# Optimization experiments

Hardware: AMD Instinct MI355X
Metric: run time of the kernel (lower is better)

## Reference

```python
import jax, jax.numpy as jnp
import numpy as np

# Model hyperparameters (match init_kwargs)
G = 256      # graph_size
K = 6        # conv kernel size
CH = 8       # channels
ROWS = 4
COLS = 3
B = 64       # batch
H = G - K + 1  # conv output side (square) = 251


def setup_inputs() -> dict:
    key = jax.random.key(0)
    k1, k2, k3, k4 = jax.random.split(key, 4)
    x = jax.random.normal(k1, (B, G, G), dtype=jnp.float32)
    # Conv2d(1, CH, (K,K)) weights, kaiming_normal_ (fan_in = 1*K*K, gain=sqrt(2))
    fan_in = 1 * K * K
    conv_w = jax.random.normal(k2, (CH, 1, K, K), dtype=jnp.float32) * np.float32(np.sqrt(2.0 / fan_in))
    # torch Conv2d default bias init: U(-1/sqrt(fan_in), 1/sqrt(fan_in))
    bound = np.float32(1.0 / np.sqrt(fan_in))
    conv_b = jax.random.uniform(k3, (CH,), dtype=jnp.float32, minval=-bound, maxval=bound)
    # coef parameter [CH, ROWS, COLS], kaiming_normal_ (fan_in = ROWS*COLS)
    coef = jax.random.normal(k4, (CH, ROWS, COLS), dtype=jnp.float32) * np.float32(np.sqrt(2.0 / (ROWS * COLS)))
    return {"x": x, "conv_w": conv_w, "conv_b": conv_b, "coef": coef}


def _traces_of_powers(C):
    """C: [H,H]. Returns traces of C^(i+2) for i in 0..ROWS-1 (matches torch loop:
    x_series[0]=C@C; at step i it records trace(x_series[i]) = trace(C^(i+2))."""
    def step(P, _):
        return C @ P, jnp.trace(P)
    _, ts = jax.lax.scan(step, C @ C, None, length=ROWS)
    return ts  # [ROWS]


def reference(x, conv_w, conv_b, coef):
    # conv over each sample treated as [1,1,G,G] -> vectorized as [B,1,G,G]
    y = jax.lax.conv_general_dilated(
        x[:, None], conv_w, window_strides=(1, 1), padding='VALID',
        dimension_numbers=('NCHW', 'OIHW', 'NCHW'))
    y = y + conv_b[None, :, None, None]           # [B, CH, H, H]

    ts = jax.vmap(jax.vmap(_traces_of_powers))(y)  # [B, CH, ROWS]

    jpow = jnp.arange(1, COLS + 1, dtype=jnp.float32)            # exponents j+1
    ret = ts[..., None] ** jpow                                  # [B, CH, ROWS, COLS]
    numel = jnp.float32(H * H)
    exps = (jnp.arange(ROWS, dtype=jnp.float32)[:, None]
            + jnp.arange(COLS, dtype=jnp.float32)[None, :] + 1.0)  # i+j+1
    ret = ret / (numel ** exps)                                  # [B, CH, ROWS, COLS]

    terms = coef[None] * ret
    return terms.sum(axis=(1, 2, 3))  # [B]
```

## Files before the change

### kernel.cpp

```cpp
#include <hip/hip_runtime.h>

typedef short short8 __attribute__((ext_vector_type(8)));
typedef float f32x4 __attribute__((ext_vector_type(4)));

#define B_    64
#define CH_   8
#define NBC   512
#define MATU  65536
#define H_    251
#define PADX  73
#define LDSW  40

__device__ inline unsigned short bf16r(float f){
    unsigned u = __float_as_uint(f);
    u += 0x7fffu + ((u >> 16) & 1u);
    return (unsigned short)(u >> 16);
}
__device__ inline float bf16f(unsigned short h){ return __uint_as_float(((unsigned)h) << 16); }
__device__ inline unsigned packsplit(float v){
    unsigned short h = bf16r(v);
    unsigned short l = bf16r(v - bf16f(h));
    return (((unsigned)h) << 16) | (unsigned)l;
}
__device__ inline float unpackf(unsigned u){
    return __uint_as_float(u & 0xffff0000u) + bf16f((unsigned short)(u & 0xffffu));
}

__global__ __launch_bounds__(256) void conv_pack(const float* __restrict__ x,
                                                 const float* __restrict__ w,
                                                 const float* __restrict__ bias,
                                                 unsigned* __restrict__ Ypk,
                                                 int b_base) {
    __shared__ float xt[69 * PADX];
    __shared__ float wsm[76];

    int tid = threadIdx.x;
    int tile = blockIdx.x;
    int lb = blockIdx.y;
    int cp = blockIdx.z;
    int b = b_base + lb;
    int r0 = (tile >> 2) * 64, c0 = (tile & 3) * 64;

    if (tid < 72) wsm[tid] = w[cp * 72 + tid];
    if (tid < 2)  wsm[72 + tid] = bias[cp * 2 + tid];

    const float* xb = x + (size_t)b * 65536;
    for (int idx = tid; idx < 69 * PADX; idx += 256) {
        int row = idx / PADX, col = idx - row * PADX;
        float v = 0.f;
        if (col < 69) {
            int gr = r0 + row; if (gr > 255) gr = 255;
            int gc = c0 + col; if (gc > 255) gc = 255;
            v = xb[gr * 256 + gc];
        }
        xt[idx] = v;
    }
    __syncthreads();

    int tx = tid & 15, ty = tid >> 4;

    for (int cc = 0; cc < 2; ++cc) {
        int ch = cp * 2 + cc;
        float acc[4][4];
        float bv = wsm[72 + cc];
        #pragma unroll
        for (int i = 0; i < 4; ++i)
            #pragma unroll
            for (int j = 0; j < 4; ++j) acc[i][j] = bv;

        const float* wc = &wsm[cc * 36];
        #pragma unroll
        for (int ir = 0; ir < 9; ++ir) {
            float row[9];
            #pragma unroll
            for (int c = 0; c < 9; ++c) row[c] = xt[(ty * 4 + ir) * PADX + tx * 4 + c];
            #pragma unroll
            for (int i = 0; i < 4; ++i) {
                int u = ir - i;
                if (u >= 0 && u < 6) {
                    #pragma unroll
                    for (int v = 0; v < 6; ++v) {
                        float wv = wc[u * 6 + v];
                        #pragma unroll
                        for (int j = 0; j < 4; ++j) acc[i][j] += row[j + v] * wv;
                    }
                }
            }
        }

        unsigned pk[4][4];
        #pragma unroll
        for (int i = 0; i < 4; ++i) {
            int gr = r0 + ty * 4 + i;
            #pragma unroll
            for (int j = 0; j < 4; ++j) {
                int gc = c0 + tx * 4 + j;
                float v = (gr < H_ && gc < H_) ? acc[i][j] : 0.f;
                pk[i][j] = packsplit(v);
            }
        }

        unsigned* yrow = Ypk + (size_t)(lb * 8 + ch) * MATU;
        #pragma unroll
        for (int i = 0; i < 4; ++i) {
            uint4 v = make_uint4(pk[i][0], pk[i][1], pk[i][2], pk[i][3]);
            *(uint4*)&yrow[(size_t)(r0 + ty * 4 + i) * 256 + c0 + tx * 4] = v;
        }
    }
}

template<int PHASE>
__global__ __launch_bounds__(256) void gemm_mfma(const unsigned* __restrict__ Apk,
                                                 const unsigned* __restrict__ Ypk,
                                                 unsigned* __restrict__ Mpk,
                                                 double* __restrict__ pdiag,
                                                 double* __restrict__ pfull,
                                                 int bc_base, int cur) {
    __shared__ __align__(16) char smem[53248];
    __shared__ double redbuf[8];

    unsigned short* Ahi = (unsigned short*)smem;
    unsigned short* Alo = (unsigned short*)(smem + 10240);
    unsigned short* Bhi = (unsigned short*)(smem + 20480);
    unsigned short* Blo = (unsigned short*)(smem + 36864);

    int tid = threadIdx.x;

    int hw = blockIdx.x;
    int xcd = hw & 7, s = hw >> 3;
    int mpx = cur >> 3;
    int lbc = xcd * mpx + (s >> 2);
    int t4 = s & 3;
    int by = t4 >> 1, bx = t4 & 1;
    int bi = by * 128, bj = bx * 128;
    int bc = bc_base + lbc;

    const unsigned* A = Apk + (size_t)lbc * MATU;

    int wid = tid >> 6, l = tid & 63;
    int wr = wid >> 1, wc = wid & 1;
    int l15 = l & 15, lk = l >> 4;

    f32x4 acc[4][4];
    #pragma unroll
    for (int m = 0; m < 4; ++m)
        #pragma unroll
        for (int n = 0; n < 4; ++n) acc[m][n] = (f32x4){0.f, 0.f, 0.f, 0.f};

    const int cl  = tid & 31;
    const int grp = tid >> 5;
    const int kq  = grp * 4;
    const int kb  = grp >> 1;
    const int koff = (grp & 1) * 4;

    for (int k0 = 0; k0 < 256; k0 += 32) {
        #pragma unroll
        for (int p = 0; p < 4; ++p) {
            int g = p * 256 + tid;
            int row = g >> 3, chn = g & 7;
            uint4 qa = *(const uint4*)(A + (size_t)(bi + row) * 256 + k0 + chn * 4);
            *(ushort4*)&Ahi[row * LDSW + chn * 4] =
                make_ushort4(qa.x >> 16, qa.y >> 16, qa.z >> 16, qa.w >> 16);
            *(ushort4*)&Alo[row * LDSW + chn * 4] =
                make_ushort4(qa.x & 0xffff, qa.y & 0xffff, qa.z & 0xffff, qa.w & 0xffff);
        }
        {
            const unsigned* Bp = A + (size_t)(k0 + kq) * 256 + bj + cl;
            unsigned d[4][4];
            #pragma unroll
            for (int i = 0; i < 4; ++i)
                #pragma unroll
                for (int j = 0; j < 4; ++j)
                    d[i][j] = Bp[i * 256 + j * 32];
            #pragma unroll
            for (int j = 0; j < 4; ++j) {
                int c = cl + 32 * j;
                *(ushort4*)&Bhi[kb * 1024 + c * 8 + koff] =
                    make_ushort4(d[0][j] >> 16, d[1][j] >> 16, d[2][j] >> 16, d[3][j] >> 16);
                *(ushort4*)&Blo[kb * 1024 + c * 8 + koff] =
                    make_ushort4(d[0][j] & 0xffff, d[1][j] & 0xffff, d[2][j] & 0xffff, d[3][j] & 0xffff);
            }
        }
        __syncthreads();

        short8 ah[4], al[4], bh[4], bl[4];
        #pragma unroll
        for (int m = 0; m < 4; ++m) {
            int r = wr * 64 + m * 16 + l15;
            ah[m] = *(const short8*)&Ahi[r * LDSW + lk * 8];
            al[m] = *(const short8*)&Alo[r * LDSW + lk * 8];
        }
        #pragma unroll
        for (int n = 0; n < 4; ++n) {
            int c = wc * 64 + n * 16 + l15;
            bh[n] = *(const short8*)&Bhi[lk * 1024 + c * 8];
            bl[n] = *(const short8*)&Blo[lk * 1024 + c * 8];
        }
        #pragma unroll
        for (int m = 0; m < 4; ++m)
            #pragma unroll
            for (int n = 0; n < 4; ++n) {
                acc[m][n] = __builtin_amdgcn_mfma_f32_16x16x32_bf16(ah[m], bh[n], acc[m][n], 0, 0, 0);
                acc[m][n] = __builtin_amdgcn_mfma_f32_16x16x32_bf16(ah[m], bl[n], acc[m][n], 0, 0, 0);
                acc[m][n] = __builtin_amdgcn_mfma_f32_16x16x32_bf16(al[m], bh[n], acc[m][n], 0, 0, 0);
            }
        __syncthreads();
    }

    const unsigned* Yb = Ypk + (size_t)lbc * MATU;
    unsigned* Mw = (PHASE == 1) ? (Mpk + (size_t)lbc * MATU) : nullptr;
    float s_full = 0.f, s_diag = 0.f;
    #pragma unroll
    for (int m = 0; m < 4; ++m) {
        int rg0 = bi + wr * 64 + m * 16 + lk * 4;
        #pragma unroll
        for (int n = 0; n < 4; ++n) {
            int cg = bj + wc * 64 + n * 16 + l15;
            uint4 yq = *(const uint4*)(Yb + (size_t)cg * 256 + rg0);
            unsigned yu[4] = {yq.x, yq.y, yq.z, yq.w};
            f32x4 v = acc[m][n];
            #pragma unroll
            for (int reg = 0; reg < 4; ++reg) {
                float val = v[reg];
                s_full += val * unpackf(yu[reg]);
                if (rg0 + reg == cg) s_diag += val;
                if (PHASE == 1) Mw[(size_t)(rg0 + reg) * 256 + cg] = packsplit(val);
            }
        }
    }

    double df = (double)s_full, dd = (double)s_diag;
    #pragma unroll
    for (int off = 32; off > 0; off >>= 1) {
        df += __shfl_down(df, off, 64);
        dd += __shfl_down(dd, off, 64);
    }
    __syncthreads();
    if (l == 0) { redbuf[wid] = df; redbuf[4 + wid] = dd; }
    __syncthreads();
    if (tid == 0) {
        pfull[(size_t)bc * 4 + by * 2 + bx] =
            redbuf[0] + redbuf[1] + redbuf[2] + redbuf[3];
        if (bx == by)
            pdiag[(size_t)bc * 2 + bx] =
                redbuf[4] + redbuf[5] + redbuf[6] + redbuf[7];
    }
}

__global__ void combine(const double* __restrict__ p2, const double* __restrict__ p3,
                        const double* __restrict__ p4, const double* __restrict__ p5,
                        const float* __restrict__ coef, float* __restrict__ out) {
    int b = threadIdx.x;
    if (b >= B_) return;
    const double numel = (double)(H_ * H_);
    double acc = 0.0;
    for (int ch = 0; ch < CH_; ++ch) {
        int bc = b * CH_ + ch;
        double t[4];
        t[0] = p2[bc * 2] + p2[bc * 2 + 1];
        t[1] = p3[bc * 4] + p3[bc * 4 + 1] + p3[bc * 4 + 2] + p3[bc * 4 + 3];
        t[2] = p4[bc * 2] + p4[bc * 2 + 1];
        t[3] = p5[bc * 4] + p5[bc * 4 + 1] + p5[bc * 4 + 2] + p5[bc * 4 + 3];
        double npow_i = numel;
        for (int i = 0; i < 4; ++i) {
            double tv = t[i];
            double p = tv, d = npow_i;
            for (int j = 0; j < 3; ++j) {
                acc += (double)coef[ch * 12 + i * 3 + j] * (p / d);
                p *= tv;
                d *= numel;
            }
            npow_i *= numel;
        }
    }
    out[b] = (float)acc;
}

extern "C" void kernel_launch(void* const* d_in, const int* in_sizes, int n_in,
                              void* d_out, int out_size, void* d_ws, size_t ws_size,
                              hipStream_t stream) {
    const float* x    = (const float*)d_in[0];
    const float* w    = (const float*)d_in[1];
    const float* bias = (const float*)d_in[2];
    const float* coef = (const float*)d_in[3];
    float* out = (float*)d_out;

    double* p2 = (double*)d_ws;
    double* p3 = p2 + NBC * 2;
    double* p4 = p3 + NBC * 4;
    double* p5 = p4 + NBC * 2;
    const size_t head = 65536;

    const size_t per_mat = (size_t)MATU * 4;
    size_t avail = (ws_size > head) ? ws_size - head : 0;
    int NC = (int)(avail / (2 * per_mat));
    NC &= ~7;
    if (NC > 256) NC = 256;
    if (NC < 8) NC = 8;

    unsigned* Ypk = (unsigned*)((char*)d_ws + head);
    unsigned* Mpk = Ypk + (size_t)NC * MATU;

    for (int bc0 = 0; bc0 < NBC; bc0 += NC) {
        int cur = NBC - bc0;
        if (cur > NC) cur = NC;
        int nb = cur / 8;
        conv_pack<<<dim3(16, nb, 4), 256, 0, stream>>>(x, w, bias, Ypk, bc0 / 8);
        gemm_mfma<1><<<cur * 4, 256, 0, stream>>>(Ypk, Ypk, Mpk, p2, p3, bc0, cur);
        gemm_mfma<2><<<cur * 4, 256, 0, stream>>>(Mpk, Ypk, nullptr, p4, p5, bc0, cur);
    }
    combine<<<1, 64, 0, stream>>>(p2, p3, p4, p5, coef, out);
}
```

Before: 279.2 us.

## Prefetch next GEMM k-tile into registers and compute four conv channels per block

Measured after the change: 256.2 us. 8.2% less time.

```diff
diff --git a/kernel.cpp b/kernel.cpp
--- a/kernel.cpp
+++ b/kernel.cpp
@@ -32,17 +32,17 @@
                                                  unsigned* __restrict__ Ypk,
                                                  int b_base) {
     __shared__ float xt[69 * PADX];
-    __shared__ float wsm[76];
+    __shared__ float wsm[148];
 
     int tid = threadIdx.x;
     int tile = blockIdx.x;
     int lb = blockIdx.y;
-    int cp = blockIdx.z;
+    int cq = blockIdx.z;
     int b = b_base + lb;
     int r0 = (tile >> 2) * 64, c0 = (tile & 3) * 64;
 
-    if (tid < 72) wsm[tid] = w[cp * 72 + tid];
-    if (tid < 2)  wsm[72 + tid] = bias[cp * 2 + tid];
+    if (tid < 144) wsm[tid] = w[cq * 144 + tid];
+    if (tid < 4)   wsm[144 + tid] = bias[cq * 4 + tid];
 
     const float* xb = x + (size_t)b * 65536;
     for (int idx = tid; idx < 69 * PADX; idx += 256) {
@@ -59,21 +59,24 @@
 
     int tx = tid & 15, ty = tid >> 4;
 
-    for (int cc = 0; cc < 2; ++cc) {
-        int ch = cp * 2 + cc;
-        float acc[4][4];
-        float bv = wsm[72 + cc];
+    float acc[4][4][4];
+    #pragma unroll
+    for (int cc = 0; cc < 4; ++cc) {
+        float bv = wsm[144 + cc];
         #pragma unroll
         for (int i = 0; i < 4; ++i)
             #pragma unroll
-            for (int j = 0; j < 4; ++j) acc[i][j] = bv;
-
-        const float* wc = &wsm[cc * 36];
-        #pragma unroll
-        for (int ir = 0; ir < 9; ++ir) {
-            float row[9];
-            #pragma unroll
-            for (int c = 0; c < 9; ++c) row[c] = xt[(ty * 4 + ir) * PADX + tx * 4 + c];
+            for (int j = 0; j < 4; ++j) acc[cc][i][j] = bv;
+    }
+
+    #pragma unroll
+    for (int ir = 0; ir < 9; ++ir) {
+        float row[9];
+        #pragma unroll
+        for (int c = 0; c < 9; ++c) row[c] = xt[(ty * 4 + ir) * PADX + tx * 4 + c];
+        #pragma unroll
+        for (int cc = 0; cc < 4; ++cc) {
+            const float* wc = &wsm[cc * 36];
             #pragma unroll
             for (int i = 0; i < 4; ++i) {
                 int u = ir - i;
@@ -82,12 +85,16 @@
                     for (int v = 0; v < 6; ++v) {
                         float wv = wc[u * 6 + v];
                         #pragma unroll
-                        for (int j = 0; j < 4; ++j) acc[i][j] += row[j + v] * wv;
+                        for (int j = 0; j < 4; ++j) acc[cc][i][j] += row[j + v] * wv;
                     }
                 }
             }
         }
-
+    }
+
+    #pragma unroll
+    for (int cc = 0; cc < 4; ++cc) {
+        int ch = cq * 4 + cc;
         unsigned pk[4][4];
         #pragma unroll
         for (int i = 0; i < 4; ++i) {
@@ -95,11 +102,10 @@
             #pragma unroll
             for (int j = 0; j < 4; ++j) {
                 int gc = c0 + tx * 4 + j;
-                float v = (gr < H_ && gc < H_) ? acc[i][j] : 0.f;
+                float v = (gr < H_ && gc < H_) ? acc[cc][i][j] : 0.f;
                 pk[i][j] = packsplit(v);
             }
         }
-
         unsigned* yrow = Ypk + (size_t)(lb * 8 + ch) * MATU;
         #pragma unroll
         for (int i = 0; i < 4; ++i) {
@@ -147,41 +153,60 @@
         #pragma unroll
         for (int n = 0; n < 4; ++n) acc[m][n] = (f32x4){0.f, 0.f, 0.f, 0.f};
 
+    const int arow = tid >> 3;
+    const int achn = tid & 7;
     const int cl  = tid & 31;
     const int grp = tid >> 5;
     const int kq  = grp * 4;
     const int kb  = grp >> 1;
     const int koff = (grp & 1) * 4;
 
-    for (int k0 = 0; k0 < 256; k0 += 32) {
+    uint4 qa[4];
+    unsigned d[4][4];
+
+    #pragma unroll
+    for (int p = 0; p < 4; ++p)
+        qa[p] = *(const uint4*)(A + (size_t)(bi + p * 32 + arow) * 256 + achn * 4);
+    {
+        const unsigned* Bp = A + (size_t)kq * 256 + bj + cl;
+        #pragma unroll
+        for (int i = 0; i < 4; ++i)
+            #pragma unroll
+            for (int j = 0; j < 4; ++j)
+                d[i][j] = Bp[i * 256 + j * 32];
+    }
+
+    for (int ks = 0; ks < 8; ++ks) {
         #pragma unroll
         for (int p = 0; p < 4; ++p) {
-            int g = p * 256 + tid;
-            int row = g >> 3, chn = g & 7;
-            uint4 qa = *(const uint4*)(A + (size_t)(bi + row) * 256 + k0 + chn * 4);
-            *(ushort4*)&Ahi[row * LDSW + chn * 4] =
-                make_ushort4(qa.x >> 16, qa.y >> 16, qa.z >> 16, qa.w >> 16);
-            *(ushort4*)&Alo[row * LDSW + chn * 4] =
-                make_ushort4(qa.x & 0xffff, qa.y & 0xffff, qa.z & 0xffff, qa.w & 0xffff);
-        }
-        {
-            const unsigned* Bp = A + (size_t)(k0 + kq) * 256 + bj + cl;
-            unsigned d[4][4];
+            int row = p * 32 + arow;
+            *(ushort4*)&Ahi[row * LDSW + achn * 4] =
+                make_ushort4(qa[p].x >> 16, qa[p].y >> 16, qa[p].z >> 16, qa[p].w >> 16);
+            *(ushort4*)&Alo[row * LDSW + achn * 4] =
+                make_ushort4(qa[p].x & 0xffff, qa[p].y & 0xffff, qa[p].z & 0xffff, qa[p].w & 0xffff);
+        }
+        #pragma unroll
+        for (int j = 0; j < 4; ++j) {
+            int c = cl + 32 * j;
+            *(ushort4*)&Bhi[kb * 1024 + c * 8 + koff] =
+                make_ushort4(d[0][j] >> 16, d[1][j] >> 16, d[2][j] >> 16, d[3][j] >> 16);
+            *(ushort4*)&Blo[kb * 1024 + c * 8 + koff] =
+                make_ushort4(d[0][j] & 0xffff, d[1][j] & 0xffff, d[2][j] & 0xffff, d[3][j] & 0xffff);
+        }
+        __syncthreads();
+
+        if (ks < 7) {
+            int k1 = (ks + 1) * 32;
+            #pragma unroll
+            for (int p = 0; p < 4; ++p)
+                qa[p] = *(const uint4*)(A + (size_t)(bi + p * 32 + arow) * 256 + k1 + achn * 4);
+            const unsigned* Bp = A + (size_t)(k1 + kq) * 256 + bj + cl;
             #pragma unroll
             for (int i = 0; i < 4; ++i)
                 #pragma unroll
                 for (int j = 0; j < 4; ++j)
                     d[i][j] = Bp[i * 256 + j * 32];
-            #pragma unroll
-            for (int j = 0; j < 4; ++j) {
-                int c = cl + 32 * j;
-                *(ushort4*)&Bhi[kb * 1024 + c * 8 + koff] =
-                    make_ushort4(d[0][j] >> 16, d[1][j] >> 16, d[2][j] >> 16, d[3][j] >> 16);
-                *(ushort4*)&Blo[kb * 1024 + c * 8 + koff] =
-                    make_ushort4(d[0][j] & 0xffff, d[1][j] & 0xffff, d[2][j] & 0xffff, d[3][j] & 0xffff);
-            }
-        }
-        __syncthreads();
+        }
 
         short8 ah[4], al[4], bh[4], bl[4];
         #pragma unroll
@@ -305,7 +330,7 @@
         int cur = NBC - bc0;
         if (cur > NC) cur = NC;
         int nb = cur / 8;
-        conv_pack<<<dim3(16, nb, 4), 256, 0, stream>>>(x, w, bias, Ypk, bc0 / 8);
+        conv_pack<<<dim3(16, nb, 2), 256, 0, stream>>>(x, w, bias, Ypk, bc0 / 8);
         gemm_mfma<1><<<cur * 4, 256, 0, stream>>>(Ypk, Ypk, Mpk, p2, p3, bc0, cur);
         gemm_mfma<2><<<cur * 4, 256, 0, stream>>>(Mpk, Ypk, nullptr, p4, p5, bc0, cur);
     }
```
